# Optimization experiments

Measured on AMD Instinct MI355X. Metric: run time of the kernel, lower is better.

## Reference

```python
import jax, jax.numpy as jnp
import numpy as np

B, T, E, L, N, V = 512, 1005, 100, 10, 20, 32000


def prelu(x, a):
    return jnp.where(x >= 0, x, a * x)


def setup_inputs() -> dict:
    key = jax.random.key(0)
    ks = jax.random.split(key, 11)
    s = 0.1  # ~xavier std for 100x100
    return {
        "in_data": jax.random.normal(ks[0], (B, T, E), dtype=jnp.float32),
        "f": jax.random.normal(ks[1], (L, E), dtype=jnp.float32) * s,
        "h0": jax.random.normal(ks[2], (1, N, E), dtype=jnp.float32) * s,
        "w_mem": jax.random.normal(ks[3], (1, N, E), dtype=jnp.float32) * s,
        "U_w": jax.random.normal(ks[4], (E, E), dtype=jnp.float32) * s,
        "V_w": jax.random.normal(ks[5], (E, E), dtype=jnp.float32) * s,
        "W_w": jax.random.normal(ks[6], (E, E), dtype=jnp.float32) * s,
        "a_dm": jnp.full((1,), 0.25, dtype=jnp.float32),
        "H_w": jax.random.normal(ks[7], (E, E), dtype=jnp.float32) * s,
        "H_b": jax.random.normal(ks[8], (E,), dtype=jnp.float32) * s,
        "R_w": jax.random.normal(ks[9], (V, E), dtype=jnp.float32) * s,
        "R_b": jax.random.normal(ks[10], (V,), dtype=jnp.float32) * s,
        "a_out": jnp.full((1,), 0.25, dtype=jnp.float32),
    }


def reference(in_data, f, h0, w_mem, U_w, V_w, W_w, a_dm, H_w, H_b, R_w, R_b, a_out):
    n_full = T // L  # rest = T % L != 0 by construction -> torch loop runs n_full times
    rest = T % L
    # InputEncoder over all full sentences at once: [B, n_full, E]
    chunks = in_data[:, : n_full * L].reshape(B, n_full, L, E)
    infos = jnp.einsum("le,bnle->bne", f, chunks)
    # precompute V(w) term (constant across steps): [1, N, E]
    Vw = jnp.einsum("one,fe->onf", w_mem, V_w)

    def step(h, s):  # h: [B,N,E], s: [B,E]
        g = jax.nn.sigmoid(jnp.einsum("bne,be->bn", h + w_mem, s))[..., None]
        cand = prelu(
            jnp.einsum("bne,fe->bnf", h, U_w)
            + Vw
            + jnp.einsum("be,fe->bf", s, W_w)[:, None, :],
            a_dm,
        )
        h = h + g * cand
        h = h / jnp.linalg.norm(h, axis=2, keepdims=True)
        return h, None

    h_init = jnp.broadcast_to(h0, (B, N, E))
    h, _ = jax.lax.scan(step, h_init, jnp.swapaxes(infos, 0, 1))  # scan over sentences

    # query = InputEncoder on trailing remainder tokens
    q_tok = in_data[:, n_full * L :]  # [B, rest, E]
    q = jnp.einsum("le,ble->be", f[:rest], q_tok)  # [B, E]

    # OutputModule
    p = jax.nn.softmax(jnp.einsum("bne,be->bn", h, q), axis=1)  # [B, N]
    u = jnp.einsum("bn,bne->be", p, h)  # [B, E]
    y = q + u @ H_w.T + H_b
    return prelu(y, a_out) @ R_w.T + R_b  # [B, V]
```

## Files before the change

kernel.cpp:

```cpp
#include <hip/hip_runtime.h>
#include <hip/hip_bf16.h>

#define E      100
#define E2     112
#define NSLOT  20
#define BB     512
#define TT     1005
#define NFULL  100
#define LL     10
#define REST   5
#define VV     32000

typedef _Float16 f16x8 __attribute__((ext_vector_type(8)));
typedef _Float16 f16x4 __attribute__((ext_vector_type(4)));
typedef float    f32x16 __attribute__((ext_vector_type(16)));

__global__ __launch_bounds__(256) void k_cvt(
    const float* __restrict__ R_w, const float* __restrict__ W_w,
    const float* __restrict__ w_mem,
    _Float16* __restrict__ R16, _Float16* __restrict__ Wm16)
{
    const int gid = blockIdx.x * 256 + threadIdx.x;
    {
        int v = gid / 28, e4 = gid % 28;
        f16x4 o;
        if (e4 < 25) {
            float4 x = *(const float4*)&R_w[(size_t)v * E + e4 * 4];
            o[0] = (_Float16)x.x; o[1] = (_Float16)x.y;
            o[2] = (_Float16)x.z; o[3] = (_Float16)x.w;
        } else { o[0] = o[1] = o[2] = o[3] = (_Float16)0.f; }
        *(f16x4*)&R16[(size_t)v * E2 + e4 * 4] = o;
    }
    if (gid < 128 * 28) {
        int j = gid / 28, e4 = gid % 28;
        f16x4 o; o[0] = o[1] = o[2] = o[3] = (_Float16)0.f;
        if (e4 < 25 && j < 120) {
            float4 x = (j < 100) ? *(const float4*)&W_w[j * E + e4 * 4]
                                 : *(const float4*)&w_mem[(j - 100) * E + e4 * 4];
            o[0] = (_Float16)x.x; o[1] = (_Float16)x.y;
            o[2] = (_Float16)x.z; o[3] = (_Float16)x.w;
        }
        *(f16x4*)&Wm16[j * E2 + e4 * 4] = o;
    }
}

__global__ __launch_bounds__(256, 2) void k_prep(
    const float* __restrict__ in_data, const float* __restrict__ f,
    _Float16* __restrict__ s16, float* __restrict__ q_all)
{
    __shared__ float4 f4s[250];
    const int tid = threadIdx.x;
    const int b   = blockIdx.x;
    if (tid < 250) f4s[tid] = ((const float4*)f)[tid];
    __syncthreads();

    const size_t base = (size_t)b * TT * E;
    for (int idx = tid; idx < 2500; idx += 256) {
        int n = idx / 25, e4 = idx - n * 25;
        float4 a; a.x = a.y = a.z = a.w = 0.f;
        const float* xp = in_data + base + (size_t)(n * LL) * E + e4 * 4;
        #pragma unroll
        for (int l = 0; l < LL; ++l) {
            float4 x = *(const float4*)(xp + l * E);
            float4 fv = f4s[l * 25 + e4];
            a.x += fv.x * x.x; a.y += fv.y * x.y;
            a.z += fv.z * x.z; a.w += fv.w * x.w;
        }
        f16x4 o;
        o[0] = (_Float16)a.x; o[1] = (_Float16)a.y;
        o[2] = (_Float16)a.z; o[3] = (_Float16)a.w;
        *(f16x4*)&s16[((size_t)n * BB + b) * E2 + e4 * 4] = o;
    }
    for (int idx = tid; idx < 600; idx += 256) {
        int n = idx / 6, k = idx - n * 6;
        ((unsigned int*)s16)[(((size_t)n * BB + b) * E2 + 100) / 2 + k] = 0u;
    }
    if (tid < E) {
        const float* fp = (const float*)f4s;
        float a = 0.f;
        #pragma unroll
        for (int l = 0; l < REST; ++l)
            a += fp[l * E + tid] * in_data[base + (size_t)(NFULL * LL + l) * E + tid];
        q_all[(size_t)b * E + tid] = a;
    }
}

__global__ __launch_bounds__(256, 2) void k_mm(
    const _Float16* __restrict__ s16, const _Float16* __restrict__ Wm16,
    _Float16* __restrict__ sws16)
{
    __shared__ __align__(16) _Float16 AF[14 * 128 * 8];
    __shared__ __align__(16) _Float16 BF[14 * 128 * 8];
    const int tid  = threadIdx.x;
    const int mb   = blockIdx.x;
    const int lane = tid & 63;
    const int wv   = tid >> 6;
    const int half = lane >> 5;
    const int jt   = wv * 32 + (lane & 31);

    for (int idx = tid; idx < 128 * 14; idx += 256) {
        int m = idx / 14, c8 = idx - m * 14;
        *(f16x8*)&AF[(c8 * 128 + m) * 8] =
            *(const f16x8*)&s16[((size_t)mb * 128 + m) * E2 + c8 * 8];
        *(f16x8*)&BF[(c8 * 128 + m) * 8] =
            *(const f16x8*)&Wm16[m * E2 + c8 * 8];
    }
    __syncthreads();

    f16x8 Bfr[7];
    #pragma unroll
    for (int ck = 0; ck < 7; ++ck)
        Bfr[ck] = *(const f16x8*)&BF[((ck * 2 + half) * 128 + jt) * 8];

    #pragma unroll
    for (int Mt = 0; Mt < 4; ++Mt) {
        f32x16 acc;
        #pragma unroll
        for (int r = 0; r < 16; ++r) acc[r] = 0.f;
        #pragma unroll
        for (int ck = 0; ck < 7; ++ck) {
            f16x8 a = *(const f16x8*)&AF[((ck * 2 + half) * 128 + 32 * Mt + (lane & 31)) * 8];
            acc = __builtin_amdgcn_mfma_f32_32x32x16_f16(a, Bfr[ck], acc, 0, 0, 0);
        }
        #pragma unroll
        for (int r = 0; r < 16; ++r) {
            int row = 32 * Mt + (r & 3) + 8 * (r >> 2) + 4 * half;
            sws16[((size_t)mb * 128 + row) * 128 + jt] = (_Float16)acc[r];
        }
    }
}

#define BAR() do { asm volatile("s_waitcnt lgkmcnt(0)" ::: "memory"); \
                   __builtin_amdgcn_s_barrier(); } while (0)

__global__ __launch_bounds__(256, 2) void k_scan(
    const float* __restrict__ h0, const float* __restrict__ w_mem,
    const float* __restrict__ U_w, const float* __restrict__ V_w,
    const float* __restrict__ a_dm,
    const _Float16* __restrict__ s16, const _Float16* __restrict__ sws16,
    float* __restrict__ h_final)
{
    __shared__ __align__(16) _Float16 h16f[7 * 64 * 8];
    __shared__ __align__(16) _Float16 svL[2][128];
    __shared__ __align__(16) _Float16 swsL[2][128];
    __shared__ __align__(16) float2   nggL[32];

    const int tid  = threadIdx.x;
    const int b    = blockIdx.x;
    const int lane = tid & 63;
    const int wv   = tid >> 6;
    const int col  = lane & 31;
    const int half = lane >> 5;
    const float adm = a_dm[0];

    int wb[4];
    #pragma unroll
    for (int q = 0; q < 4; ++q) {
        int eq = 32 * wv + 4 * half + 8 * q;
        int bp = (eq >> 3) * 512 + col * 16 + 8 * half;
        wb[q] = bp ^ (((bp >> 9) & 3) << 5);
    }
    int rb[7];
    #pragma unroll
    for (int ck = 0; ck < 7; ++ck) {
        int bp = ck * 1024 + lane * 16;
        rb[ck] = bp ^ (((bp >> 9) & 3) << 5);
    }

    f16x8 Uf[7];
    const int fA = 32 * wv + col;
    #pragma unroll
    for (int ck = 0; ck < 7; ++ck) {
        #pragma unroll
        for (int j = 0; j < 8; ++j) {
            int e = 16 * ck + 8 * half + j;
            Uf[ck][j] = (_Float16)((fA < E && e < E) ? U_w[fA * E + e] : 0.f);
        }
    }
    float VwC[16], hC[16];
    #pragma unroll
    for (int r = 0; r < 16; ++r) { VwC[r] = 0.f; hC[r] = 0.f; }
    for (int e4 = 0; e4 < 25; ++e4) {
        float4 w4 = make_float4(0.f, 0.f, 0.f, 0.f);
        if (col < NSLOT) w4 = *(const float4*)&w_mem[col * E + e4 * 4];
        #pragma unroll
        for (int r = 0; r < 16; ++r) {
            int f = 32 * wv + (r & 3) + 8 * (r >> 2) + 4 * half;
            if (f < E) {
                float4 v4 = *(const float4*)&V_w[f * E + e4 * 4];
                VwC[r] += w4.x * v4.x + w4.y * v4.y + w4.z * v4.z + w4.w * v4.w;
            }
        }
    }
    #pragma unroll
    for (int r = 0; r < 16; ++r) {
        int f = 32 * wv + (r & 3) + 8 * (r >> 2) + 4 * half;
        if (col < NSLOT && f < E) hC[r] = h0[col * E + f];
    }
    for (int idx = tid; idx < 896; idx += 256)
        ((float2*)h16f)[idx] = make_float2(0.f, 0.f);
    __syncthreads();
    if (col < NSLOT) {
        #pragma unroll
        for (int q = 0; q < 4; ++q) {
            int f0 = 32 * wv + 4 * half + 8 * q;
            if (f0 < E) {
                f16x4 pk;
                #pragma unroll
                for (int i = 0; i < 4; ++i) pk[i] = (_Float16)hC[4 * q + i];
                *(f16x4*)((char*)h16f + wb[q]) = pk;
            }
        }
    }
    if (tid < E2) svL[0][tid] = s16[(size_t)b * E2 + tid];
    else if (tid >= 128) swsL[0][tid - 128] = sws16[(size_t)b * 128 + (tid - 128)];
    BAR();

    const unsigned short* s16u   = (const unsigned short*)s16;
    const unsigned short* sws16u = (const unsigned short*)sws16;

    for (int t = 0; t < NFULL; ++t) {
        const int p = t & 1;

        unsigned short nsv = 0, nsw = 0;
        if (t + 1 < NFULL) {
            if (tid < E2) nsv = s16u[((size_t)(t + 1) * BB + b) * E2 + tid];
            else if (tid >= 128) nsw = sws16u[((size_t)(t + 1) * BB + b) * 128 + (tid - 128)];
        }
        if (wv == 3 && col == 4) {
            #pragma unroll
            for (int ck = 0; ck < 7; ++ck)
                Uf[ck] = *(const f16x8*)&svL[p][16 * ck + 8 * half];
        }
        f16x8 hB[7];
        #pragma unroll
        for (int ck = 0; ck < 7; ++ck)
            hB[ck] = *(const f16x8*)((const char*)h16f + rb[ck]);

        f32x16 acc;
        #pragma unroll
        for (int r = 0; r < 16; ++r) acc[r] = 0.f;
        #pragma unroll
        for (int ck = 0; ck < 7; ++ck)
            acc = __builtin_amdgcn_mfma_f32_32x32x16_f16(Uf[ck], hB[ck], acc, 0, 0, 0);

        if (wv == 1) {
            f32x16 acc2;
            #pragma unroll
            for (int r = 0; r < 16; ++r) acc2[r] = 0.f;
            #pragma unroll
            for (int ck = 0; ck < 7; ++ck)
                acc2 = __builtin_amdgcn_mfma_f32_32x32x16_f16(hB[ck], hB[ck], acc2, 0, 0, 0);
            #pragma unroll
            for (int r = 0; r < 16; ++r) {
                int rp = (r & 3) + 8 * (r >> 2) + 4 * half;
                if (rp == col) nggL[col].x = acc2[r];
            }
        }
        if (wv == 3 && half == 1) nggL[col].y = acc[0];
        BAR();

        float2 ng = nggL[col];
        float rn = (t == 0) ? 1.f : __builtin_amdgcn_rsqf(ng.x);
        float dd = fmaf(rn, ng.y, (float)swsL[p][100 + col]);
        float g  = __builtin_amdgcn_rcpf(1.f + __expf(-dd));

        if (col < NSLOT) {
            #pragma unroll
            for (int q = 0; q < 4; ++q) {
                int f0 = 32 * wv + 4 * half + 8 * q;
                if (f0 < E) {
                    f16x4 sw4 = *(const f16x4*)&swsL[p][f0];
                    f16x4 pk;
                    #pragma unroll
                    for (int i = 0; i < 4; ++i) {
                        int r = 4 * q + i;
                        float c = fmaf(rn, acc[r], VwC[r] + (float)sw4[i]);
                        c = (c >= 0.f) ? c : adm * c;
                        float hnew = fmaf(rn, hC[r], g * c);
                        hC[r] = hnew;
                        pk[i] = (_Float16)hnew;
                    }
                    *(f16x4*)((char*)h16f + wb[q]) = pk;
                }
            }
        }
        if (t + 1 < NFULL) {
            int pn = p ^ 1;
            if (tid < E2) ((unsigned short*)svL[pn])[tid] = nsv;
            else if (tid >= 128) ((unsigned short*)swsL[pn])[tid - 128] = nsw;
        }
        BAR();
    }

    {
        if (wv == 1) {
            f16x8 hB[7];
            #pragma unroll
            for (int ck = 0; ck < 7; ++ck)
                hB[ck] = *(const f16x8*)((const char*)h16f + rb[ck]);
            f32x16 acc2;
            #pragma unroll
            for (int r = 0; r < 16; ++r) acc2[r] = 0.f;
            #pragma unroll
            for (int ck = 0; ck < 7; ++ck)
                acc2 = __builtin_amdgcn_mfma_f32_32x32x16_f16(hB[ck], hB[ck], acc2, 0, 0, 0);
            #pragma unroll
            for (int r = 0; r < 16; ++r) {
                int rp = (r & 3) + 8 * (r >> 2) + 4 * half;
                if (rp == col) nggL[col].x = acc2[r];
            }
        }
        BAR();
        float rn = __builtin_amdgcn_rsqf(nggL[col].x);
        if (col < NSLOT) {
            #pragma unroll
            for (int q = 0; q < 4; ++q) {
                int f0 = 32 * wv + 4 * half + 8 * q;
                if (f0 < E) {
                    float4 o;
                    o.x = rn * hC[4 * q + 0];
                    o.y = rn * hC[4 * q + 1];
                    o.z = rn * hC[4 * q + 2];
                    o.w = rn * hC[4 * q + 3];
                    *(float4*)&h_final[(size_t)b * NSLOT * E + col * E + f0] = o;
                }
            }
        }
    }
}

__global__ __launch_bounds__(256, 2) void k_attn(
    const float* __restrict__ h_final, const float* __restrict__ q_all,
    const float* __restrict__ H_w, const float* __restrict__ H_b,
    const float* __restrict__ a_out, _Float16* __restrict__ py16)
{
    __shared__ float Hl[E * 101];
    __shared__ float h_l[NSLOT * E];
    __shared__ float q_l[E], u_l[E];
    __shared__ float part[200], party[200];
    __shared__ float dl[NSLOT], pl[NSLOT];
    const int tid = threadIdx.x;
    const int b   = blockIdx.x;

    for (int idx = tid; idx < E * E; idx += 256) {
        int fr = idx / E, e = idx - fr * E;
        Hl[fr * 101 + e] = H_w[idx];
    }
    for (int idx = tid; idx < NSLOT * E; idx += 256)
        h_l[idx] = h_final[(size_t)b * NSLOT * E + idx];
    if (tid < E) q_l[tid] = q_all[(size_t)b * E + tid];
    __syncthreads();

    if (tid < 200) {
        int n = tid / 10, j = tid - n * 10;
        float a = 0.f;
        #pragma unroll
        for (int k = 0; k < 10; ++k) { int e = j * 10 + k; a += h_l[n * E + e] * q_l[e]; }
        part[tid] = a;
    }
    __syncthreads();
    if (tid < NSLOT) {
        float d = 0.f;
        #pragma unroll
        for (int j = 0; j < 10; ++j) d += part[tid * 10 + j];
        dl[tid] = d;
    }
    __syncthreads();
    if (tid < NSLOT) {
        float m = -1e30f;
        for (int i = 0; i < NSLOT; ++i) m = fmaxf(m, dl[i]);
        float s = 0.f;
        for (int i = 0; i < NSLOT; ++i) s += __expf(dl[i] - m);
        pl[tid] = __expf(dl[tid] - m) / s;
    }
    __syncthreads();
    if (tid < E) {
        float u = 0.f;
        for (int n = 0; n < NSLOT; ++n) u += pl[n] * h_l[n * E + tid];
        u_l[tid] = u;
    }
    __syncthreads();
    if (tid < 200) {
        int fr = tid % E, hf = tid / E;
        float a = 0.f;
        for (int e = hf * 50; e < hf * 50 + 50; ++e) a += u_l[e] * Hl[fr * 101 + e];
        party[tid] = a;
    }
    __syncthreads();
    if (tid < E2) {
        if (tid < E) {
            float y = q_l[tid] + H_b[tid] + party[tid] + party[100 + tid];
            const float ao = a_out[0];
            y = (y >= 0.f) ? y : ao * y;
            py16[(size_t)b * E2 + tid] = (_Float16)y;
        } else py16[(size_t)b * E2 + tid] = (_Float16)0.f;
    }
}

__global__ __launch_bounds__(256, 2) void k_out(
    const _Float16* __restrict__ py16, const _Float16* __restrict__ R16,
    const float* __restrict__ R_b, float* __restrict__ out)
{
    __shared__ __align__(16) _Float16 AF[14 * 128 * 8];
    __shared__ __align__(16) _Float16 BF[14 * 128 * 8];
    const int tid  = threadIdx.x;
    const int vb   = blockIdx.x;
    const int mb   = blockIdx.y;
    const int lane = tid & 63;
    const int wv   = tid >> 6;
    const int half = lane >> 5;
    const int jt   = wv * 32 + (lane & 31);
    const int v0   = vb * 128;

    for (int idx = tid; idx < 128 * 14; idx += 256) {
        int m = idx / 14, c8 = idx - m * 14;
        *(f16x8*)&AF[(c8 * 128 + m) * 8] =
            *(const f16x8*)&py16[((size_t)mb * 128 + m) * E2 + c8 * 8];
        *(f16x8*)&BF[(c8 * 128 + m) * 8] =
            *(const f16x8*)&R16[(size_t)(v0 + m) * E2 + c8 * 8];
    }
    __syncthreads();

    f16x8 Bfr[7];
    #pragma unroll
    for (int ck = 0; ck < 7; ++ck)
        Bfr[ck] = *(const f16x8*)&BF[((ck * 2 + half) * 128 + jt) * 8];
    const float rbv = R_b[v0 + jt];

    #pragma unroll
    for (int Mt = 0; Mt < 4; ++Mt) {
        f32x16 acc;
        #pragma unroll
        for (int r = 0; r < 16; ++r) acc[r] = 0.f;
        #pragma unroll
        for (int ck = 0; ck < 7; ++ck) {
            f16x8 a = *(const f16x8*)&AF[((ck * 2 + half) * 128 + 32 * Mt + (lane & 31)) * 8];
            acc = __builtin_amdgcn_mfma_f32_32x32x16_f16(a, Bfr[ck], acc, 0, 0, 0);
        }
        #pragma unroll
        for (int r = 0; r < 16; ++r) {
            int row = 32 * Mt + (r & 3) + 8 * (r >> 2) + 4 * half;
            out[((size_t)mb * 128 + row) * VV + v0 + jt] = acc[r] + rbv;
        }
    }
}

extern "C" void kernel_launch(void* const* d_in, const int* in_sizes, int n_in,
                              void* d_out, int out_size, void* d_ws, size_t ws_size,
                              hipStream_t stream)
{
    const float* in_data = (const float*)d_in[0];
    const float* f       = (const float*)d_in[1];
    const float* h0      = (const float*)d_in[2];
    const float* w_mem   = (const float*)d_in[3];
    const float* U_w     = (const float*)d_in[4];
    const float* V_w     = (const float*)d_in[5];
    const float* W_w     = (const float*)d_in[6];
    const float* a_dm    = (const float*)d_in[7];
    const float* H_w     = (const float*)d_in[8];
    const float* H_b     = (const float*)d_in[9];
    const float* R_w     = (const float*)d_in[10];
    const float* R_b     = (const float*)d_in[11];
    const float* a_out   = (const float*)d_in[12];
    float* out = (float*)d_out;

    char* ws = (char*)d_ws;
    _Float16* s16    = (_Float16*)(ws);
    _Float16* sws16  = (_Float16*)(ws + 11468800);
    _Float16* R16    = (_Float16*)(ws + 24576000);
    _Float16* Wm16   = (_Float16*)(ws + 31744000);
    float*    q_all  = (float*)   (ws + 31772672);
    float*    h_fin  = (float*)   (ws + 31977472);
    _Float16* py16   = (_Float16*)(ws + 36073472);

    k_cvt <<<3500, 256, 0, stream>>>(R_w, W_w, w_mem, R16, Wm16);
    k_prep<<<BB, 256, 0, stream>>>(in_data, f, s16, q_all);
    k_mm  <<<400, 256, 0, stream>>>(s16, Wm16, sws16);
    k_scan<<<BB, 256, 0, stream>>>(h0, w_mem, U_w, V_w, a_dm, s16, sws16, h_fin);
    k_attn<<<BB, 256, 0, stream>>>(h_fin, q_all, H_w, H_b, a_out, py16);
    k_out <<<dim3(VV / 128, 4), 256, 0, stream>>>(py16, R16, R_b, out);
}
```

Before: 594.1 us.

## Double-buffer h in LDS, drop mid-step barrier, compute norms redundantly per wave

The recurrent scan kernel now keeps two LDS copies of the packed fp16 state, reading one and writing the other, so each timestep needs one barrier instead of two. Every wave computes the Gram diagonal (h·h) and the gate dot product itself with an extra MFMA chain and a cross-half shuffle, instead of one wave writing them to shared memory. The per-step input vectors now go from global memory straight into registers and into a spare column of the h buffer, replacing the separate LDS staging arrays. In exchange, each wave issues twice the MFMAs and holds more registers, and the LDS footprint grows.

```diff
diff --git a/kernel.cpp b/kernel.cpp
--- a/kernel.cpp
+++ b/kernel.cpp
@@ -140,10 +140,7 @@
     const _Float16* __restrict__ s16, const _Float16* __restrict__ sws16,
     float* __restrict__ h_final)
 {
-    __shared__ __align__(16) _Float16 h16f[7 * 64 * 8];
-    __shared__ __align__(16) _Float16 svL[2][128];
-    __shared__ __align__(16) _Float16 swsL[2][128];
-    __shared__ __align__(16) float2   nggL[32];
+    __shared__ __align__(16) _Float16 h16f[2][7 * 64 * 8];
 
     const int tid  = threadIdx.x;
     const int b    = blockIdx.x;
@@ -152,12 +149,12 @@
     const int col  = lane & 31;
     const int half = lane >> 5;
     const float adm = a_dm[0];
+    const int cg   = (col < NSLOT) ? col : 0;
 
     int wb[4];
     #pragma unroll
     for (int q = 0; q < 4; ++q) {
-        int eq = 32 * wv + 4 * half + 8 * q;
-        int bp = (eq >> 3) * 512 + col * 16 + 8 * half;
+        int bp = (4 * wv + q) * 512 + col * 16 + 8 * half;
         wb[q] = bp ^ (((bp >> 9) & 3) << 5);
     }
     int rb[7];
@@ -197,7 +194,7 @@
         int f = 32 * wv + (r & 3) + 8 * (r >> 2) + 4 * half;
         if (col < NSLOT && f < E) hC[r] = h0[col * E + f];
     }
-    for (int idx = tid; idx < 896; idx += 256)
+    for (int idx = tid; idx < 1792; idx += 256)
         ((float2*)h16f)[idx] = make_float2(0.f, 0.f);
     __syncthreads();
     if (col < NSLOT) {
@@ -208,111 +205,136 @@
                 f16x4 pk;
                 #pragma unroll
                 for (int i = 0; i < 4; ++i) pk[i] = (_Float16)hC[4 * q + i];
-                *(f16x4*)((char*)h16f + wb[q]) = pk;
+                *(f16x4*)((char*)h16f[0] + wb[q]) = pk;
             }
         }
-    }
-    if (tid < E2) svL[0][tid] = s16[(size_t)b * E2 + tid];
-    else if (tid >= 128) swsL[0][tid - 128] = sws16[(size_t)b * 128 + (tid - 128)];
-    BAR();
-
-    const unsigned short* s16u   = (const unsigned short*)s16;
-    const unsigned short* sws16u = (const unsigned short*)sws16;
+    } else if (col == NSLOT) {
+        #pragma unroll
+        for (int q = 0; q < 4; ++q) {
+            int f0 = 32 * wv + 4 * half + 8 * q;
+            if (f0 < E)
+                *(f16x4*)((char*)h16f[0] + wb[q]) =
+                    *(const f16x4*)&s16[(size_t)b * E2 + f0];
+        }
+    }
+    f16x4 cur_sw[4];
+    _Float16 cur_swn;
+    {
+        const size_t r0 = (size_t)b * 128;
+        #pragma unroll
+        for (int q = 0; q < 4; ++q) {
+            int f0 = 32 * wv + 4 * half + 8 * q;
+            if (f0 < E) cur_sw[q] = *(const f16x4*)&sws16[r0 + f0];
+            else { cur_sw[q][0] = cur_sw[q][1] = cur_sw[q][2] = cur_sw[q][3] = (_Float16)0.f; }
+        }
+        cur_swn = sws16[r0 + 100 + cg];
+    }
+    __syncthreads();
 
     for (int t = 0; t < NFULL; ++t) {
         const int p = t & 1;
 
-        unsigned short nsv = 0, nsw = 0;
-        if (t + 1 < NFULL) {
-            if (tid < E2) nsv = s16u[((size_t)(t + 1) * BB + b) * E2 + tid];
-            else if (tid >= 128) nsw = sws16u[((size_t)(t + 1) * BB + b) * 128 + (tid - 128)];
-        }
-        if (wv == 3 && col == 4) {
+        const int tn = (t + 1 < NFULL) ? (t + 1) : t;
+        const size_t rown = (size_t)tn * BB + b;
+        f16x4 nxt_sw[4], nxt_s[4];
+        _Float16 nxt_swn;
+        #pragma unroll
+        for (int q = 0; q < 4; ++q) {
+            int f0 = 32 * wv + 4 * half + 8 * q;
+            if (f0 < E) nxt_sw[q] = *(const f16x4*)&sws16[rown * 128 + f0];
+            else { nxt_sw[q][0] = nxt_sw[q][1] = nxt_sw[q][2] = nxt_sw[q][3] = (_Float16)0.f; }
+        }
+        nxt_swn = sws16[rown * 128 + 100 + cg];
+        if (col == NSLOT) {
             #pragma unroll
-            for (int ck = 0; ck < 7; ++ck)
-                Uf[ck] = *(const f16x8*)&svL[p][16 * ck + 8 * half];
-        }
+            for (int q = 0; q < 4; ++q) {
+                int f0 = 32 * wv + 4 * half + 8 * q;
+                if (f0 < E) nxt_s[q] = *(const f16x4*)&s16[rown * E2 + f0];
+            }
+        }
+
+        const char* hb = (const char*)h16f[p];
         f16x8 hB[7];
         #pragma unroll
         for (int ck = 0; ck < 7; ++ck)
-            hB[ck] = *(const f16x8*)((const char*)h16f + rb[ck]);
-
-        f32x16 acc;
-        #pragma unroll
-        for (int r = 0; r < 16; ++r) acc[r] = 0.f;
-        #pragma unroll
-        for (int ck = 0; ck < 7; ++ck)
-            acc = __builtin_amdgcn_mfma_f32_32x32x16_f16(Uf[ck], hB[ck], acc, 0, 0, 0);
-
-        if (wv == 1) {
-            f32x16 acc2;
-            #pragma unroll
-            for (int r = 0; r < 16; ++r) acc2[r] = 0.f;
-            #pragma unroll
-            for (int ck = 0; ck < 7; ++ck)
-                acc2 = __builtin_amdgcn_mfma_f32_32x32x16_f16(hB[ck], hB[ck], acc2, 0, 0, 0);
-            #pragma unroll
-            for (int r = 0; r < 16; ++r) {
-                int rp = (r & 3) + 8 * (r >> 2) + 4 * half;
-                if (rp == col) nggL[col].x = acc2[r];
-            }
-        }
-        if (wv == 3 && half == 1) nggL[col].y = acc[0];
-        BAR();
-
-        float2 ng = nggL[col];
-        float rn = (t == 0) ? 1.f : __builtin_amdgcn_rsqf(ng.x);
-        float dd = fmaf(rn, ng.y, (float)swsL[p][100 + col]);
+            hB[ck] = *(const f16x8*)(hb + rb[ck]);
+
+        f32x16 acc, acc2;
+        #pragma unroll
+        for (int r = 0; r < 16; ++r) { acc[r] = 0.f; acc2[r] = 0.f; }
+        #pragma unroll
+        for (int ck = 0; ck < 7; ++ck) {
+            acc  = __builtin_amdgcn_mfma_f32_32x32x16_f16(Uf[ck], hB[ck], acc,  0, 0, 0);
+            acc2 = __builtin_amdgcn_mfma_f32_32x32x16_f16(hB[ck], hB[ck], acc2, 0, 0, 0);
+        }
+
+        float nv = 0.f;
+        #pragma unroll
+        for (int r = 0; r < 16; ++r) {
+            const int row = (r & 3) + 8 * (r >> 2) + 4 * half;
+            if (row == col) nv = acc2[r];
+        }
+        float gv = half ? acc2[8] : 0.f;
+        nv += __shfl_xor(nv, 32);
+        gv += __shfl_xor(gv, 32);
+
+        float rn = (t == 0) ? 1.f : __builtin_amdgcn_rsqf(nv);
+        float dd = fmaf(rn, gv, (float)cur_swn);
         float g  = __builtin_amdgcn_rcpf(1.f + __expf(-dd));
 
+        char* hw = (char*)h16f[p ^ 1];
         if (col < NSLOT) {
             #pragma unroll
             for (int q = 0; q < 4; ++q) {
                 int f0 = 32 * wv + 4 * half + 8 * q;
                 if (f0 < E) {
-                    f16x4 sw4 = *(const f16x4*)&swsL[p][f0];
                     f16x4 pk;
                     #pragma unroll
                     for (int i = 0; i < 4; ++i) {
                         int r = 4 * q + i;
-                        float c = fmaf(rn, acc[r], VwC[r] + (float)sw4[i]);
+                        float c = fmaf(rn, acc[r], VwC[r] + (float)cur_sw[q][i]);
                         c = (c >= 0.f) ? c : adm * c;
                         float hnew = fmaf(rn, hC[r], g * c);
                         hC[r] = hnew;
                         pk[i] = (_Float16)hnew;
                     }
-                    *(f16x4*)((char*)h16f + wb[q]) = pk;
+                    *(f16x4*)(hw + wb[q]) = pk;
                 }
             }
-        }
-        if (t + 1 < NFULL) {
-            int pn = p ^ 1;
-            if (tid < E2) ((unsigned short*)svL[pn])[tid] = nsv;
-            else if (tid >= 128) ((unsigned short*)swsL[pn])[tid - 128] = nsw;
-        }
+        } else if (col == NSLOT) {
+            #pragma unroll
+            for (int q = 0; q < 4; ++q) {
+                int f0 = 32 * wv + 4 * half + 8 * q;
+                if (f0 < E) *(f16x4*)(hw + wb[q]) = nxt_s[q];
+            }
+        }
+        #pragma unroll
+        for (int q = 0; q < 4; ++q) cur_sw[q] = nxt_sw[q];
+        cur_swn = nxt_swn;
+
         BAR();
     }
 
     {
-        if (wv == 1) {
-            f16x8 hB[7];
-            #pragma unroll
-            for (int ck = 0; ck < 7; ++ck)
-                hB[ck] = *(const f16x8*)((const char*)h16f + rb[ck]);
-            f32x16 acc2;
-            #pragma unroll
-            for (int r = 0; r < 16; ++r) acc2[r] = 0.f;
-            #pragma unroll
-            for (int ck = 0; ck < 7; ++ck)
-                acc2 = __builtin_amdgcn_mfma_f32_32x32x16_f16(hB[ck], hB[ck], acc2, 0, 0, 0);
-            #pragma unroll
-            for (int r = 0; r < 16; ++r) {
-                int rp = (r & 3) + 8 * (r >> 2) + 4 * half;
-                if (rp == col) nggL[col].x = acc2[r];
-            }
-        }
-        BAR();
-        float rn = __builtin_amdgcn_rsqf(nggL[col].x);
+        const char* hb = (const char*)h16f[0];
+        f16x8 hB[7];
+        #pragma unroll
+        for (int ck = 0; ck < 7; ++ck)
+            hB[ck] = *(const f16x8*)(hb + rb[ck]);
+        f32x16 acc2;
+        #pragma unroll
+        for (int r = 0; r < 16; ++r) acc2[r] = 0.f;
+        #pragma unroll
+        for (int ck = 0; ck < 7; ++ck)
+            acc2 = __builtin_amdgcn_mfma_f32_32x32x16_f16(hB[ck], hB[ck], acc2, 0, 0, 0);
+        float nv = 0.f;
+        #pragma unroll
+        for (int r = 0; r < 16; ++r) {
+            const int row = (r & 3) + 8 * (r >> 2) + 4 * half;
+            if (row == col) nv = acc2[r];
+        }
+        nv += __shfl_xor(nv, 32);
+        float rn = __builtin_amdgcn_rsqf(nv);
         if (col < NSLOT) {
             #pragma unroll
             for (int q = 0; q < 4; ++q) {
```

After: 581.9 us. 1.02x faster.
